# Performance work log

Hardware: AMD Instinct MI355X
Metric: run time of the kernel (lower is better)

Reference implementation:

```python
import jax, jax.numpy as jnp
import numpy as np

B, T, X, E, H, L = 4096, 32, 256, 32, 512, 2  # batch, theta_size, x_size, n_masks, hidden, num_hidden_layers


def _prelu(v, a):
    # PReLU with per-channel slope a (broadcast [E,H] or [B,E,H] vs [B,E,H])
    return jnp.where(v >= 0, v, a * v)


def setup_inputs() -> dict:
    key = jax.random.key(0)
    ks = jax.random.split(key, 12)
    theta = jax.random.normal(ks[0], (B, T), dtype=jnp.float32)
    x = jax.random.normal(ks[1], (B, X), dtype=jnp.float32)
    masks = jax.random.randint(ks[2], (E, T), 0, 2, dtype=jnp.int32)
    masks = masks.at[:, 0].set(1)  # guarantee non-empty subsets
    D = T + X
    s_in = 1.0 / np.sqrt(D)
    s_h = 1.0 / np.sqrt(H)
    # first Linear, split into theta-part and x-part of the weight matrix
    W1t = jax.random.normal(ks[3], (E, T, H), dtype=jnp.float32) * s_in
    W1x = jax.random.normal(ks[4], (E, X, H), dtype=jnp.float32) * s_in
    b1 = jax.random.normal(ks[5], (E, H), dtype=jnp.float32) * s_in
    a1 = jnp.full((E, H), 0.25, dtype=jnp.float32)  # PReLU init
    # num_layers hidden Linear(H,H) + PReLU
    Wh = jax.random.normal(ks[6], (L, E, H, H), dtype=jnp.float32) * s_h
    bh = jax.random.normal(ks[7], (L, E, H), dtype=jnp.float32) * s_h
    ah = jnp.full((L, E, H), 0.25, dtype=jnp.float32)
    # output Linear(H, 1) -> squeeze(-1)
    Wo = jax.random.normal(ks[8], (E, H), dtype=jnp.float32) * s_h
    bo = jax.random.normal(ks[9], (E,), dtype=jnp.float32) * s_h
    return {"theta": theta, "x": x, "masks": masks, "W1t": W1t, "W1x": W1x,
            "b1": b1, "a1": a1, "Wh": Wh, "bh": bh, "ah": ah, "Wo": Wo, "bo": bo}


def reference(theta, x, masks, W1t, W1x, b1, a1, Wh, bh, ah, Wo, bo):
    # theta[..., mask] followed by Linear is equivalent to masking theta per
    # expert and contracting with the full per-expert theta weight block.
    m = masks.astype(theta.dtype)                      # [E, T]
    tm = theta[:, None, :] * m[None, :, :]             # [B, E, T]
    h = (jnp.einsum('bet,eth->beh', tm, W1t)
         + jnp.einsum('bx,exh->beh', x, W1x) + b1)     # [B, E, H]
    h = _prelu(h, a1)
    for i in range(Wh.shape[0]):                       # small fixed layer loop
        h = jnp.einsum('beh,ehk->bek', h, Wh[i]) + bh[i]
        h = _prelu(h, ah[i])
    # Linear(H,1).squeeze(-1), stacked over masks on the last dim -> [B, E]
    return jnp.einsum('beh,eh->be', h, Wo) + bo
```

## Files before the change

kernel.cpp:

```cpp
#include <hip/hip_runtime.h>
#include <stdint.h>

#define B_SZ 4096
#define T_SZ 32
#define X_SZ 256
#define E_SZ 32
#define H_SZ 512
#define BM   64
#define AROW 1040

typedef __attribute__((ext_vector_type(8))) short  short8;
typedef __attribute__((ext_vector_type(4))) float  floatx4;

__device__ __forceinline__ unsigned short f2bf(float f) {
  unsigned u = __float_as_uint(f);
  u += 0x7fffu + ((u >> 16) & 1u);
  return (unsigned short)(u >> 16);
}
__device__ __forceinline__ unsigned pk2(float a, float b) {
  return (unsigned)f2bf(a) | ((unsigned)f2bf(b) << 16);
}

__global__ __launch_bounds__(256) void prep_kernel(
    const float* __restrict__ W1t, const float* __restrict__ W1x,
    const int* __restrict__ masks, const float* __restrict__ Wh,
    uint4* __restrict__ wcat, uint4* __restrict__ whf) {
  int gid = blockIdx.x * 256 + threadIdx.x;
  const int NU1 = E_SZ * 9 * 2048;
  if (gid < NU1) {
    int c  = gid >> 11;
    int u  = gid & 2047;
    int e  = c / 9, kt = c - e * 9;
    int nb = u >> 6, l = u & 63;
    int n  = nb * 16 + (l & 15);
    int k0 = kt * 32 + (l >> 4) * 8;
    unsigned r[4];
#pragma unroll
    for (int p = 0; p < 4; ++p) {
      int   k  = k0 + p * 2;
      float v0 = (k < T_SZ)
                     ? W1t[(e * T_SZ + k) * H_SZ + n] * (float)masks[e * T_SZ + k]
                     : W1x[(e * X_SZ + (k - T_SZ)) * H_SZ + n];
      int   k1 = k + 1;
      float v1 = (k1 < T_SZ)
                     ? W1t[(e * T_SZ + k1) * H_SZ + n] * (float)masks[e * T_SZ + k1]
                     : W1x[(e * X_SZ + (k1 - T_SZ)) * H_SZ + n];
      r[p] = pk2(v0, v1);
    }
    wcat[gid] = make_uint4(r[0], r[1], r[2], r[3]);
  } else {
    int g  = gid - NU1;
    int c  = g >> 11;
    int u  = g & 2047;
    int kt = c & 15, le = c >> 4;
    int nb = u >> 6, l = u & 63;
    int n  = nb * 16 + (l & 15);
    int k0 = kt * 32 + (l >> 4) * 8;
    const float* base = Wh + (size_t)le * H_SZ * H_SZ + n;
    unsigned r[4];
#pragma unroll
    for (int p = 0; p < 4; ++p) {
      float v0 = base[(size_t)(k0 + p * 2) * H_SZ];
      float v1 = base[(size_t)(k0 + p * 2 + 1) * H_SZ];
      r[p] = pk2(v0, v1);
    }
    whf[g] = make_uint4(r[0], r[1], r[2], r[3]);
  }
}

__global__ __launch_bounds__(512, 4) void mlp_kernel(
    const float* __restrict__ theta, const float* __restrict__ x,
    const short8* __restrict__ wcat, const short8* __restrict__ whf,
    const float* __restrict__ b1, const float* __restrict__ a1,
    const float* __restrict__ bh, const float* __restrict__ ah,
    const float* __restrict__ Wo, const float* __restrict__ bo,
    float* __restrict__ out) {
  __shared__ __align__(16) char smA[BM * AROW];
  const int tid = threadIdx.x;
  const int bid = blockIdx.x;
  const int r5  = bid & 31;
  const int e   = (r5 & 7) * 4 + (r5 >> 3);
  const int m0  = (bid >> 5) * BM;
  const int w   = tid >> 6, l = tid & 63, l16 = l & 15, quad = l >> 4;

  {
    int r = tid >> 3, c = tid & 7;
    float4 th = *(const float4*)(theta + (size_t)(m0 + r) * T_SZ + c * 4);
    *(uint2*)(smA + r * AROW + c * 8) = make_uint2(pk2(th.x, th.y), pk2(th.z, th.w));
    const float4* xp = (const float4*)(x + (size_t)(m0 + r) * X_SZ + c * 32);
#pragma unroll
    for (int q = 0; q < 4; ++q) {
      float4 a = xp[q * 2], b = xp[q * 2 + 1];
      *(uint4*)(smA + r * AROW + 64 + c * 64 + q * 16) =
          make_uint4(pk2(a.x, a.y), pk2(a.z, a.w), pk2(b.x, b.y), pk2(b.z, b.w));
    }
  }
  __syncthreads();

  floatx4 acc[4][4];

  auto gemm = [&](const short8* wbase, int nkt) {
#pragma unroll
    for (int mb = 0; mb < 4; ++mb)
#pragma unroll
      for (int i = 0; i < 4; ++i) acc[mb][i] = (floatx4)(0.f);
    short8 bcur[4], bnxt[4];
    const int boff = w * 256 + l;
#pragma unroll
    for (int i = 0; i < 4; ++i) bcur[i] = wbase[boff + i * 64];
    for (int kt = 0; kt < nkt; ++kt) {
      const short8* wn = wbase + (size_t)(kt + 1 < nkt ? kt + 1 : kt) * 2048;
#pragma unroll
      for (int i = 0; i < 4; ++i) bnxt[i] = wn[boff + i * 64];
      short8 af[4];
#pragma unroll
      for (int mb = 0; mb < 4; ++mb)
        af[mb] = *(const short8*)(smA + (mb * 16 + l16) * AROW + kt * 64 + quad * 16);
#pragma unroll
      for (int mb = 0; mb < 4; ++mb)
#pragma unroll
        for (int i = 0; i < 4; ++i)
          acc[mb][i] = __builtin_amdgcn_mfma_f32_16x16x32_bf16(af[mb], bcur[i],
                                                               acc[mb][i], 0, 0, 0);
#pragma unroll
      for (int i = 0; i < 4; ++i) bcur[i] = bnxt[i];
    }
  };

  auto epi_store = [&](const float* bias, const float* slope) {
    float bb[4], aa[4];
#pragma unroll
    for (int i = 0; i < 4; ++i) {
      int col = w * 64 + i * 16 + l16;
      bb[i] = bias[col];
      aa[i] = slope[col];
    }
    __syncthreads();
#pragma unroll
    for (int mb = 0; mb < 4; ++mb) {
#pragma unroll
      for (int i = 0; i < 4; ++i) {
        unsigned dw[4];
#pragma unroll
        for (int r = 0; r < 4; ++r) {
          float v = acc[mb][i][r] + bb[i];
          v = v >= 0.f ? v : aa[i] * v;
          float o  = __shfl_xor(v, 1, 64);
          float lo = (l16 & 1) ? o : v;
          float hi = (l16 & 1) ? v : o;
          dw[r] = pk2(lo, hi);
        }
        int col2  = w * 64 + i * 16 + (l16 & ~1);
        int rbase = (l16 & 1) * 2;
#pragma unroll
        for (int rr = 0; rr < 2; ++rr) {
          int row = mb * 16 + quad * 4 + rbase + rr;
          *(unsigned*)(smA + row * AROW + col2 * 2) = dw[rbase + rr];
        }
      }
    }
    __syncthreads();
  };

  gemm(wcat + (size_t)e * 9 * 2048, 9);
  epi_store(b1 + (size_t)e * H_SZ, a1 + (size_t)e * H_SZ);
  gemm(whf + (size_t)e * 16 * 2048, 16);
  epi_store(bh + (size_t)e * H_SZ, ah + (size_t)e * H_SZ);
  gemm(whf + (size_t)(E_SZ + e) * 16 * 2048, 16);
  {
    float bb[4], aa[4], wo[4];
#pragma unroll
    for (int i = 0; i < 4; ++i) {
      int col = w * 64 + i * 16 + l16;
      bb[i] = bh[(size_t)(E_SZ + e) * H_SZ + col];
      aa[i] = ah[(size_t)(E_SZ + e) * H_SZ + col];
      wo[i] = Wo[(size_t)e * H_SZ + col];
    }
    float ps[4][4];
#pragma unroll
    for (int mb = 0; mb < 4; ++mb)
#pragma unroll
      for (int r = 0; r < 4; ++r) ps[mb][r] = 0.f;
#pragma unroll
    for (int mb = 0; mb < 4; ++mb)
#pragma unroll
      for (int i = 0; i < 4; ++i)
#pragma unroll
        for (int r = 0; r < 4; ++r) {
          float v = acc[mb][i][r] + bb[i];
          v = v >= 0.f ? v : aa[i] * v;
          ps[mb][r] += v * wo[i];
        }
#pragma unroll
    for (int d = 1; d < 16; d <<= 1)
#pragma unroll
      for (int mb = 0; mb < 4; ++mb)
#pragma unroll
        for (int r = 0; r < 4; ++r) ps[mb][r] += __shfl_xor(ps[mb][r], d, 64);
    __syncthreads();
    float* scratch = (float*)smA;
    if (l16 == 0) {
#pragma unroll
      for (int mb = 0; mb < 4; ++mb)
#pragma unroll
        for (int r = 0; r < 4; ++r)
          scratch[(mb * 16 + quad * 4 + r) * 8 + w] = ps[mb][r];
    }
    __syncthreads();
    if (tid < BM) {
      float s = 0.f;
#pragma unroll
      for (int ww = 0; ww < 8; ++ww) s += scratch[tid * 8 + ww];
      out[(size_t)(m0 + tid) * E_SZ + e] = s + bo[e];
    }
  }
}

extern "C" void kernel_launch(void* const* d_in, const int* in_sizes, int n_in,
                              void* d_out, int out_size, void* d_ws, size_t ws_size,
                              hipStream_t stream) {
  const float* theta = (const float*)d_in[0];
  const float* x     = (const float*)d_in[1];
  const int*   masks = (const int*)d_in[2];
  const float* W1t   = (const float*)d_in[3];
  const float* W1x   = (const float*)d_in[4];
  const float* b1    = (const float*)d_in[5];
  const float* a1    = (const float*)d_in[6];
  const float* Wh    = (const float*)d_in[7];
  const float* bh    = (const float*)d_in[8];
  const float* ah    = (const float*)d_in[9];
  const float* Wo    = (const float*)d_in[10];
  const float* bo    = (const float*)d_in[11];
  float* out = (float*)d_out;

  uint4* wcat = (uint4*)d_ws;
  uint4* whf  = (uint4*)((char*)d_ws + (size_t)E_SZ * 9 * 2048 * 16);

  prep_kernel<<<10496, 256, 0, stream>>>(W1t, W1x, masks, Wh, wcat, whf);
  mlp_kernel<<<2048, 512, 0, stream>>>(theta, x, (const short8*)wcat,
                                       (const short8*)whf, b1, a1, bh, ah, Wo, bo,
                                       out);
}
```

Before: 323.9 us.

## Stage weight prep through LDS, use hardware bf16 pack, remap blocks per XCD

The weight-prep kernel now gives each block one 32xK-by-512 tile. The tile is read with coalesced float4 loads, packed to bf16 into LDS, and then written out in the MFMA fragment layout. This replaces strided scalar global reads. Float-to-bf16 packing now uses the v_cvt_pk_bf16_f32 instruction instead of manual rounding. The MLP kernel's block-to-(expert, row tile) mapping is changed so that all row tiles of an expert land on the same XCD, which is meant to improve L2 reuse of that expert's weights. This assumes round-robin dispatch of blocks across XCDs.

```diff
diff --git a/kernel.cpp b/kernel.cpp
--- a/kernel.cpp
+++ b/kernel.cpp
@@ -12,59 +12,66 @@
 typedef __attribute__((ext_vector_type(8))) short  short8;
 typedef __attribute__((ext_vector_type(4))) float  floatx4;
 
-__device__ __forceinline__ unsigned short f2bf(float f) {
-  unsigned u = __float_as_uint(f);
-  u += 0x7fffu + ((u >> 16) & 1u);
-  return (unsigned short)(u >> 16);
-}
 __device__ __forceinline__ unsigned pk2(float a, float b) {
-  return (unsigned)f2bf(a) | ((unsigned)f2bf(b) << 16);
+  unsigned r;
+  asm("v_cvt_pk_bf16_f32 %0, %1, %2" : "=v"(r) : "v"(a), "v"(b));
+  return r;
 }
 
 __global__ __launch_bounds__(256) void prep_kernel(
     const float* __restrict__ W1t, const float* __restrict__ W1x,
     const int* __restrict__ masks, const float* __restrict__ Wh,
     uint4* __restrict__ wcat, uint4* __restrict__ whf) {
-  int gid = blockIdx.x * 256 + threadIdx.x;
-  const int NU1 = E_SZ * 9 * 2048;
-  if (gid < NU1) {
-    int c  = gid >> 11;
-    int u  = gid & 2047;
-    int e  = c / 9, kt = c - e * 9;
-    int nb = u >> 6, l = u & 63;
-    int n  = nb * 16 + (l & 15);
-    int k0 = kt * 32 + (l >> 4) * 8;
-    unsigned r[4];
-#pragma unroll
-    for (int p = 0; p < 4; ++p) {
-      int   k  = k0 + p * 2;
-      float v0 = (k < T_SZ)
-                     ? W1t[(e * T_SZ + k) * H_SZ + n] * (float)masks[e * T_SZ + k]
-                     : W1x[(e * X_SZ + (k - T_SZ)) * H_SZ + n];
-      int   k1 = k + 1;
-      float v1 = (k1 < T_SZ)
-                     ? W1t[(e * T_SZ + k1) * H_SZ + n] * (float)masks[e * T_SZ + k1]
-                     : W1x[(e * X_SZ + (k1 - T_SZ)) * H_SZ + n];
-      r[p] = pk2(v0, v1);
-    }
-    wcat[gid] = make_uint4(r[0], r[1], r[2], r[3]);
+  __shared__ unsigned lds[16 * 516];
+  const int c = blockIdx.x;
+  const int t = threadIdx.x;
+
+  const float* base;
+  bool needMask = false;
+  int e1 = 0;
+  if (c >= 288) {
+    int cc = c - 288;
+    int le = cc >> 4, kt = cc & 15;
+    base = Wh + ((size_t)le * H_SZ + kt * 32) * H_SZ;
   } else {
-    int g  = gid - NU1;
-    int c  = g >> 11;
-    int u  = g & 2047;
-    int kt = c & 15, le = c >> 4;
-    int nb = u >> 6, l = u & 63;
-    int n  = nb * 16 + (l & 15);
-    int k0 = kt * 32 + (l >> 4) * 8;
-    const float* base = Wh + (size_t)le * H_SZ * H_SZ + n;
-    unsigned r[4];
-#pragma unroll
-    for (int p = 0; p < 4; ++p) {
-      float v0 = base[(size_t)(k0 + p * 2) * H_SZ];
-      float v1 = base[(size_t)(k0 + p * 2 + 1) * H_SZ];
-      r[p] = pk2(v0, v1);
-    }
-    whf[g] = make_uint4(r[0], r[1], r[2], r[3]);
+    int e = c / 9, kt = c - e * 9;
+    e1 = e;
+    if (kt == 0) { base = W1t + (size_t)e * T_SZ * H_SZ; needMask = true; }
+    else          base = W1x + ((size_t)e * X_SZ + (kt - 1) * 32) * H_SZ;
+  }
+
+#pragma unroll
+  for (int i = 0; i < 8; ++i) {
+    int g  = i * 256 + t;
+    int k2 = g >> 7, np = g & 127;
+    const float* r0 = base + (size_t)(2 * k2) * H_SZ + np * 4;
+    float4 a = *(const float4*)r0;
+    float4 b = *(const float4*)(r0 + H_SZ);
+    if (needMask) {
+      float s0 = (float)masks[e1 * T_SZ + 2 * k2];
+      float s1 = (float)masks[e1 * T_SZ + 2 * k2 + 1];
+      a.x *= s0; a.y *= s0; a.z *= s0; a.w *= s0;
+      b.x *= s1; b.y *= s1; b.z *= s1; b.w *= s1;
+    }
+    *(uint4*)&lds[k2 * 516 + np * 4] =
+        make_uint4(pk2(a.x, b.x), pk2(a.y, b.y), pk2(a.z, b.z), pk2(a.w, b.w));
+  }
+  __syncthreads();
+
+  uint4* outp = (c < 288) ? (wcat + (size_t)c * 2048)
+                          : (whf + (size_t)(c - 288) * 2048);
+  const int w = t >> 6, l = t & 63, q = l >> 4, l16 = l & 15;
+#pragma unroll
+  for (int j = 0; j < 8; ++j) {
+    int nb = w * 8 + j;
+    int n  = nb * 16 + l16;
+    int kb = 4 * q;
+    uint4 v;
+    v.x = lds[(kb + 0) * 516 + n];
+    v.y = lds[(kb + 1) * 516 + n];
+    v.z = lds[(kb + 2) * 516 + n];
+    v.w = lds[(kb + 3) * 516 + n];
+    outp[nb * 64 + l] = v;
   }
 }
 
@@ -78,9 +85,10 @@
   __shared__ __align__(16) char smA[BM * AROW];
   const int tid = threadIdx.x;
   const int bid = blockIdx.x;
-  const int r5  = bid & 31;
-  const int e   = (r5 & 7) * 4 + (r5 >> 3);
-  const int m0  = (bid >> 5) * BM;
+  const int xcd = bid & 7;
+  const int t8  = bid >> 3;
+  const int e   = xcd * 4 + (t8 >> 6);
+  const int m0  = (t8 & 63) * BM;
   const int w   = tid >> 6, l = tid & 63, l16 = l & 15, quad = l >> 4;
 
   {
@@ -236,7 +244,7 @@
   uint4* wcat = (uint4*)d_ws;
   uint4* whf  = (uint4*)((char*)d_ws + (size_t)E_SZ * 9 * 2048 * 16);
 
-  prep_kernel<<<10496, 256, 0, stream>>>(W1t, W1x, masks, Wh, wcat, whf);
+  prep_kernel<<<1312, 256, 0, stream>>>(W1t, W1x, masks, Wh, wcat, whf);
   mlp_kernel<<<2048, 512, 0, stream>>>(theta, x, (const short8*)wcat,
                                        (const short8*)whf, b1, a1, bh, ah, Wo, bo,
                                        out);
```

Measured after the change: 319.0 us. Within noise of the previous version (-1.5%).
